# Optimization experiments

Measured on AMD Instinct MI355X. Metric: run time of the kernel, lower is better.

Reference implementation:

```python
import jax, jax.numpy as jnp
from jax import lax
import numpy as np

EPS = 1e-5
STRIDE = 4
K_NEIGHBORS = 16


def setup_inputs() -> dict:
    key = jax.random.key(0)
    ks = jax.random.split(key, 4)
    B, N, Cin, Cout = 16, 4096, 64, 128
    p1 = jax.random.normal(ks[0], (B, N, 3), dtype=jnp.float32)
    x1 = jax.random.normal(ks[1], (B, Cin, N), dtype=jnp.float32)
    w1 = jax.random.normal(ks[2], (Cout, Cin + 3), dtype=jnp.float32) * 0.05
    w2 = jax.random.normal(ks[3], (Cout, Cout), dtype=jnp.float32) * 0.05
    g1 = jnp.ones((Cout,), jnp.float32)
    b1 = jnp.zeros((Cout,), jnp.float32)
    g2 = jnp.ones((Cout,), jnp.float32)
    b2 = jnp.zeros((Cout,), jnp.float32)
    return {"p1": p1, "x1": x1, "w1": w1, "g1": g1, "b1": b1,
            "w2": w2, "g2": g2, "b2": b2}


def farthest_point_sampling(p, npoint):
    # p: [B, N, 3] -> centroids [B, npoint] (deterministic start at index 0)
    B, N, _ = p.shape
    gather_pt = jax.vmap(lambda pts, f: pts[f])  # [B,N,3],[B] -> [B,3]

    def step(carry, _):
        dist, farthest = carry
        centroid = gather_pt(p, farthest)                     # [B, 3]
        d = jnp.sum((p - centroid[:, None, :]) ** 2, -1)      # [B, N]
        dist = jnp.minimum(dist, d)
        new_far = jnp.argmax(dist, axis=-1).astype(jnp.int32)
        return (dist, new_far), farthest

    init = (jnp.full((B, N), 1e10, dtype=p.dtype), jnp.zeros((B,), jnp.int32))
    _, idxs = lax.scan(step, init, None, length=npoint)       # [npoint, B]
    return idxs.T                                             # [B, npoint]


def knn_point(k, xyz, new_xyz):
    # squared distances via gram trick; exclude all-zero points like the original
    n1 = jnp.sum(xyz ** 2, -1)                                # [B, N]
    n2 = jnp.sum(new_xyz ** 2, -1)                            # [B, M]
    d2 = n2[:, :, None] + n1[:, None, :] - 2.0 * jnp.einsum('bmc,bnc->bmn', new_xyz, xyz)
    zero_mask = jnp.all(xyz == 0, axis=-1)                    # [B, N]
    d2 = jnp.where(zero_mask[:, None, :], jnp.inf, d2)
    _, idx = lax.top_k(-d2, k)                                # smallest-k -> [B, M, k]
    return idx


def _bn_relu(h, g, b):
    # BatchNorm2d (training-mode batch stats, biased var) over (B, M, k) per channel
    m = jnp.mean(h, axis=(0, 1, 2), keepdims=True)
    v = jnp.mean((h - m) ** 2, axis=(0, 1, 2), keepdims=True)
    return jax.nn.relu(g * (h - m) * lax.rsqrt(v + EPS) + b)


def reference(p1, x1, w1, g1, b1, w2, g2, b2):
    B, N, _ = p1.shape
    M = max(1, N // STRIDE)
    k = K_NEIGHBORS

    idx = farthest_point_sampling(p1, M)                      # [B, M]
    gather2 = jax.vmap(lambda pts, i: pts[i])
    p2 = gather2(p1, idx)                                     # [B, M, 3]

    idx_knn = knn_point(k, p1, p2)                            # [B, M, k]
    grouped_p1 = gather2(p1, idx_knn)                         # [B, M, k, 3]
    xt = jnp.transpose(x1, (0, 2, 1))                         # [B, N, Cin]
    grouped_x1 = gather2(xt, idx_knn)                         # [B, M, k, Cin]

    rel = grouped_p1 - p2[:, :, None, :]                      # [B, M, k, 3]
    feats = jnp.concatenate([rel, grouped_x1], axis=-1)       # [B, M, k, 3+Cin]

    h = _bn_relu(jnp.einsum('bmkc,oc->bmko', feats, w1), g1, b1)
    h = _bn_relu(jnp.einsum('bmkc,oc->bmko', h, w2), g2, b2)
    new_features = jnp.max(h, axis=2)                         # maxpool over k -> [B, M, Cout]
    return p2, jnp.transpose(new_features, (0, 2, 1))         # ([B,M,3], [B,Cout,M])
```

## Files before the change

### kernel.cpp

```cpp
#include <hip/hip_runtime.h>
#include <hip/hip_bf16.h>
#include <hip/hip_cooperative_groups.h>
#include <cstdint>

namespace cg = cooperative_groups;

#define BB 16
#define NN 4096
#define MM 1024
#define KNB 16
#define CIN 64
#define COUT 128
#define RTOT (BB*MM*KNB)
#define AP1 104
#define AP2 136

typedef __attribute__((ext_vector_type(8))) short short8v;
typedef __attribute__((ext_vector_type(4))) float floatx4;
typedef __attribute__((ext_vector_type(2))) float f32x2;

__device__ __forceinline__ float bflo(uint32_t u){ return __uint_as_float(u << 16); }
__device__ __forceinline__ float bfhi(uint32_t u){ return __uint_as_float(u & 0xffff0000u); }
__device__ __forceinline__ uint32_t f2bf_pk(float a, float b){
  uint32_t ua = __float_as_uint(a), ub = __float_as_uint(b);
  ua += 0x7fffu + ((ua >> 16) & 1u);
  ub += 0x7fffu + ((ub >> 16) & 1u);
  return (ua >> 16) | (ub & 0xffff0000u);
}
__device__ __forceinline__ uint16_t f2bf1(float a){
  uint32_t u = __float_as_uint(a);
  u += 0x7fffu + ((u >> 16) & 1u);
  return (uint16_t)(u >> 16);
}
template<int CTRL>
__device__ __forceinline__ float dpp_f(float v){
  return __int_as_float(__builtin_amdgcn_update_dpp(__float_as_int(v), __float_as_int(v), CTRL, 0xf, 0xf, false));
}

struct FpsS { float pc[NN*3]; float4 sel[MM]; unsigned long long cand[2][8]; };
struct TrS  { float t[64][65]; };
struct ConsS{ uint16_t Bh1[128*AP1]; uint16_t AhD[128*AP2];
              int winq[8*16]; float ssum[128]; float ssq[128]; };
union PreU  { FpsS fps; TrS tr; ConsS cons; };

__global__ __launch_bounds__(512, 2) void k_pre2(
    const float* __restrict__ p1, const float* __restrict__ x1,
    const float* __restrict__ w1,
    float* __restrict__ outp2, float* __restrict__ p2w,
    float4* __restrict__ p1n, uint16_t* __restrict__ xtb, float* __restrict__ Sz,
    uint16_t* __restrict__ h1, float* __restrict__ S1,
    int* __restrict__ prog, int* __restrict__ prep_done)
{
  __shared__ PreU u;
  const int blk = blockIdx.x, tid = threadIdx.x;
  const int lane = tid & 63, wid = tid >> 6;

  if (blk < 16){
    int b = blk;
    const float* pb = p1 + (size_t)b*NN*3;
    float4 f[6];
    const float4* src = (const float4*)(pb + tid*24);
    #pragma unroll
    for (int j=0;j<6;j++) f[j] = src[j];
    #pragma unroll
    for (int j=0;j<6;j++) *(float4*)(u.fps.pc + tid*24 + j*4) = f[j];
    const float* fa = (const float*)f;
    f32x2 px2[4], py2[4], pz2[4], ds2[4];
    #pragma unroll
    for (int j=0;j<4;j++){
      px2[j][0]=fa[6*j+0]; px2[j][1]=fa[6*j+3];
      py2[j][0]=fa[6*j+1]; py2[j][1]=fa[6*j+4];
      pz2[j][0]=fa[6*j+2]; pz2[j][1]=fa[6*j+5];
      ds2[j][0]=1e10f;     ds2[j][1]=1e10f;
    }
    __syncthreads();
    float cx = u.fps.pc[0], cy = u.fps.pc[1], cz = u.fps.pc[2];
    if (tid==64) u.fps.sel[0] = make_float4(cx, cy, cz, 0.f);
    int g0 = tid*8;

    for (int i=1;i<MM;i++){
      f32x2 nd2[4];
      {
        #pragma clang fp contract(off)
        f32x2 cx2; cx2[0]=cx; cx2[1]=cx;
        f32x2 cy2; cy2[0]=cy; cy2[1]=cy;
        f32x2 cz2; cz2[0]=cz; cz2[1]=cz;
        #pragma unroll
        for (int j=0;j<4;j++){
          f32x2 dx = px2[j] - cx2;
          f32x2 dy = py2[j] - cy2;
          f32x2 dz = pz2[j] - cz2;
          f32x2 d  = dx*dx + dy*dy + dz*dz;
          f32x2 nd;
          nd[0] = fminf(ds2[j][0], d[0]);
          nd[1] = fminf(ds2[j][1], d[1]);
          nd2[j] = nd; ds2[j] = nd;
        }
      }
      float lm = fmaxf(fmaxf(fmaxf(nd2[0][0],nd2[0][1]), fmaxf(nd2[1][0],nd2[1][1])),
                       fmaxf(fmaxf(nd2[2][0],nd2[2][1]), fmaxf(nd2[3][0],nd2[3][1])));
      int li = g0+7;
      li = (nd2[3][0]==lm) ? g0+6 : li;
      li = (nd2[2][1]==lm) ? g0+5 : li;
      li = (nd2[2][0]==lm) ? g0+4 : li;
      li = (nd2[1][1]==lm) ? g0+3 : li;
      li = (nd2[1][0]==lm) ? g0+2 : li;
      li = (nd2[0][1]==lm) ? g0+1 : li;
      li = (nd2[0][0]==lm) ? g0+0 : li;
      float wm = lm;
      wm = fmaxf(wm, dpp_f<0xB1>(wm));
      wm = fmaxf(wm, dpp_f<0x4E>(wm));
      wm = fmaxf(wm, dpp_f<0x124>(wm));
      wm = fmaxf(wm, dpp_f<0x128>(wm));
      wm = fmaxf(wm, __int_as_float(__builtin_amdgcn_ds_swizzle(__float_as_int(wm), 0x401F)));
      wm = fmaxf(wm, __shfl_xor(wm, 32));
      unsigned long long bm = __ballot(lm == wm);
      int fl = __ffsll(bm) - 1;
      int wi = __builtin_amdgcn_readlane(li, fl);
      if (lane == 0)
        u.fps.cand[i&1][wid] = (((unsigned long long)(unsigned)__float_as_uint(wm)) << 32)
                               | (unsigned)(0xFFFFu ^ (unsigned)wi);
      __syncthreads();
      const unsigned long long* cd = u.fps.cand[i&1];
      unsigned long long c0=cd[0],c1=cd[1],c2=cd[2],c3=cd[3],c4=cd[4],c5=cd[5],c6=cd[6],c7=cd[7];
      unsigned long long a0 = c0>c1?c0:c1, a1 = c2>c3?c2:c3;
      unsigned long long a2 = c4>c5?c4:c5, a3 = c6>c7?c6:c7;
      unsigned long long b0 = a0>a1?a0:a1, b1 = a2>a3?a2:a3;
      unsigned long long mb = b0>b1?b0:b1;
      int midx = (int)(0xFFFFu ^ (unsigned)(mb & 0xFFFFull));
      cx = u.fps.pc[midx*3+0]; cy = u.fps.pc[midx*3+1]; cz = u.fps.pc[midx*3+2];
      if (tid==64) u.fps.sel[i] = make_float4(cx, cy, cz, 0.f);
      if ((i & 63) == 63 && wid == 1){
        int e = i - 63 + lane;
        float4 s = u.fps.sel[e];
        float n2 = __fadd_rn(__fadd_rn(__fmul_rn(s.x,s.x),__fmul_rn(s.y,s.y)),__fmul_rn(s.z,s.z));
        *(float4*)(p2w + ((size_t)b*MM + e)*4) = make_float4(s.x, s.y, s.z, n2);
        if (lane == 0)
          __hip_atomic_store(&prog[b*16], i+1, __ATOMIC_RELEASE, __HIP_MEMORY_SCOPE_AGENT);
      }
    }
    __syncthreads();
    for (int e = tid; e < MM; e += 512){
      float4 s = u.fps.sel[e];
      float* o = outp2 + ((size_t)b*MM + e)*3;
      o[0]=s.x; o[1]=s.y; o[2]=s.z;
    }
  } else {
    for (int i = (blk-16)*512 + tid; i < 16384; i += 240*512) Sz[i] = 0.f;
    for (int i = (blk-16)*512 + tid; i < BB*NN; i += 240*512){
      float x = p1[(size_t)i*3+0], y = p1[(size_t)i*3+1], z = p1[(size_t)i*3+2];
      float n = __fadd_rn(__fadd_rn(__fmul_rn(x,x),__fmul_rn(y,y)),__fmul_rn(z,z));
      p1n[i] = make_float4(x,y,z,n);
    }
    for (int tile = blk-16; tile < 1024; tile += 240){
      int b = tile >> 6, n0 = (tile & 63)*64;
      __syncthreads();
      int c = tid >> 3, q = tid & 7;
      const float* src = x1 + ((size_t)(b*64 + c))*NN + n0 + q*8;
      float4 f0 = *(const float4*)src, f1 = *(const float4*)(src+4);
      u.tr.t[c][q*8+0]=f0.x; u.tr.t[c][q*8+1]=f0.y; u.tr.t[c][q*8+2]=f0.z; u.tr.t[c][q*8+3]=f0.w;
      u.tr.t[c][q*8+4]=f1.x; u.tr.t[c][q*8+5]=f1.y; u.tr.t[c][q*8+6]=f1.z; u.tr.t[c][q*8+7]=f1.w;
      __syncthreads();
      int n = tid >> 3;
      uint32_t* dst = (uint32_t*)(xtb + ((size_t)(b*NN + n0 + n))*64 + q*8);
      #pragma unroll
      for (int j=0;j<4;j++)
        dst[j] = f2bf_pk(u.tr.t[q*8+2*j][n], u.tr.t[q*8+2*j+1][n]);
    }
    __threadfence();
    __syncthreads();
    if (tid == 0) atomicAdd(prep_done, 1);
    for (int e = tid; e < 128*96; e += 512){
      int o = e / 96, k = e - o*96;
      float v = (k < 64) ? w1[o*67 + 3 + k] : ((k < 67) ? w1[o*67 + (k-64)] : 0.f);
      u.cons.Bh1[o*AP1 + k] = f2bf1(v);
    }
    if (tid < 128){ u.cons.ssum[tid]=0.f; u.cons.ssq[tid]=0.f; }
    __syncthreads();
    {
      int pv = 0, sp = 0;
      if (lane == 0) pv = __hip_atomic_load(prep_done, __ATOMIC_ACQUIRE, __HIP_MEMORY_SCOPE_AGENT);
      pv = __shfl(pv, 0);
      while (pv < 240 && sp < (1<<16)){
        __builtin_amdgcn_s_sleep(64);
        if (lane == 0) pv = __hip_atomic_load(prep_done, __ATOMIC_ACQUIRE, __HIP_MEMORY_SCOPE_AGENT);
        pv = __shfl(pv, 0); sp++;
      }
    }
    int ml = lane & 15, quad = lane >> 4, seg = lane >> 4;
    int gw = (blk-16)*8 + wid;
    for (int qi = gw; qi < BB*MM; qi += 1920){
      int b = qi & 15, m = qi >> 4;
      int q2 = b*MM + m;
      {
        int pv = 0, sp = 0;
        if (lane == 0) pv = __hip_atomic_load(&prog[b*16], __ATOMIC_ACQUIRE, __HIP_MEMORY_SCOPE_AGENT);
        pv = __shfl(pv, 0);
        while (pv <= m && sp < (1<<16)){
          __builtin_amdgcn_s_sleep(64);
          if (lane == 0) pv = __hip_atomic_load(&prog[b*16], __ATOMIC_ACQUIRE, __HIP_MEMORY_SCOPE_AGENT);
          pv = __shfl(pv, 0); sp++;
        }
      }
      const float4 qv = *(const float4*)(p2w + (size_t)q2*4);
      const float4* pbn = p1n + (size_t)b*NN;
      float bd[16]; int bi[16];
      #pragma unroll
      for (int s=0;s<16;s++){ bd[s] = 1e30f; bi[s] = 0; }
      float wv = 1e30f; int wslot = 0;

      #define KPROC(T, PV) { \
        float dot = fmaf(qv.z, (PV).z, fmaf(qv.y, (PV).y, __fmul_rn(qv.x, (PV).x))); \
        float d2 = __fsub_rn(__fadd_rn(qv.w, (PV).w), __fmul_rn(2.0f, dot)); \
        if (d2 < wv){ \
          int c = (T)*64 + lane; \
          _Pragma("unroll") \
          for (int s=0;s<16;s++) if (s==wslot){ bd[s]=d2; bi[s]=c; } \
          wv = bd[0]; wslot = 0; \
          _Pragma("unroll") \
          for (int s=1;s<16;s++) if (bd[s] > wv){ wv = bd[s]; wslot = s; } \
        } }

      float4 cur = pbn[lane];
      for (int t=0;t<63;t++){
        float4 nx = pbn[(t+1)*64 + lane];
        KPROC(t, cur);
        cur = nx;
      }
      KPROC(63, cur);
      #undef KPROC

      float lv = bd[0]; int ls = 0;
      #pragma unroll
      for (int s=1;s<16;s++) if (bd[s] < lv){ lv = bd[s]; ls = s; }
      for (int r=0;r<16;r++){
        float rv = lv; int rl = lane;
        #pragma unroll
        for (int off=32; off>=1; off>>=1){
          float ov = __shfl_xor(rv, off); int ol = __shfl_xor(rl, off);
          if (ov < rv || (ov == rv && ol < rl)){ rv = ov; rl = ol; }
        }
        if (lane == rl){
          int idx = 0;
          #pragma unroll
          for (int s=0;s<16;s++) if (s==ls) idx = bi[s];
          u.cons.winq[wid*16 + r] = idx;
          #pragma unroll
          for (int s=0;s<16;s++) if (s==ls) bd[s] = 1e30f;
          lv = bd[0]; ls = 0;
          #pragma unroll
          for (int s=1;s<16;s++) if (bd[s] < lv){ lv = bd[s]; ls = s; }
        }
      }
      int n = u.cons.winq[wid*16 + ml];
      {
        const uint4* s4 = (const uint4*)(xtb + ((size_t)(b*NN + n))*64 + seg*16);
        uint4* d4 = (uint4*)(u.cons.AhD + (wid*16 + ml)*AP2 + seg*16);
        d4[0] = s4[0]; d4[1] = s4[1];
        if (seg == 0){
          const float* pp = p1 + ((size_t)(b*NN + n))*3;
          float rx = __fsub_rn(pp[0], qv.x);
          float ry = __fsub_rn(pp[1], qv.y);
          float rz = __fsub_rn(pp[2], qv.z);
          uint4* dr = (uint4*)(u.cons.AhD + (wid*16 + ml)*AP2 + 64);
          dr[0] = make_uint4(f2bf_pk(rx, ry), f2bf_pk(rz, 0.f), 0u, 0u);
          dr[1] = make_uint4(0u,0u,0u,0u);
          dr[2] = make_uint4(0u,0u,0u,0u);
          dr[3] = make_uint4(0u,0u,0u,0u);
        }
      }
      short8v af[3];
      #pragma unroll
      for (int kc=0;kc<3;kc++)
        af[kc] = *(const short8v*)(u.cons.AhD + (wid*16 + ml)*AP2 + kc*32 + quad*8);
      floatx4 acc[8];
      #pragma unroll
      for (int ct=0;ct<8;ct++) acc[ct] = (floatx4){0.f,0.f,0.f,0.f};
      #pragma unroll
      for (int ct=0;ct<8;ct++){
        #pragma unroll
        for (int kc=0;kc<3;kc++){
          short8v bf = *(const short8v*)(u.cons.Bh1 + (ct*16+ml)*AP1 + kc*32 + quad*8);
          acc[ct] = __builtin_amdgcn_mfma_f32_16x16x32_bf16(af[kc], bf, acc[ct], 0, 0, 0);
        }
      }
      float csum[8], csq[8];
      #pragma unroll
      for (int ct=0;ct<8;ct++){
        float a0=acc[ct][0], a1=acc[ct][1], a2=acc[ct][2], a3=acc[ct][3];
        float s = (a0+a1)+(a2+a3);
        float qq2 = (a0*a0+a1*a1)+(a2*a2+a3*a3);
        s += __shfl_xor(s,16);  s += __shfl_xor(s,32);
        qq2 += __shfl_xor(qq2,16); qq2 += __shfl_xor(qq2,32);
        csum[ct]=s; csq[ct]=qq2;
        #pragma unroll
        for (int r=0;r<4;r++)
          u.cons.AhD[(wid*16 + quad*4 + r)*AP2 + ct*16 + ml] = f2bf1(acc[ct][r]);
      }
      #pragma unroll
      for (int jj=0;jj<2;jj++){
        int ct = quad*2 + jj, col = ct*16 + ml;
        atomicAdd(&u.cons.ssum[col], csum[ct]);
        atomicAdd(&u.cons.ssq[col],  csq[ct]);
      }
      {
        const uint4* s4 = (const uint4*)(u.cons.AhD + (wid*16 + ml)*AP2 + seg*32);
        uint4* dst = (uint4*)(h1 + ((size_t)q2*16 + ml)*128 + seg*32);
        dst[0]=s4[0]; dst[1]=s4[1]; dst[2]=s4[2]; dst[3]=s4[3];
      }
    }
    __syncthreads();
    int cp = (blk & 31)*256;
    if (tid < 128){ atomicAdd(&S1[cp+tid], u.cons.ssum[tid]); atomicAdd(&S1[cp+128+tid], u.cons.ssq[tid]); }
  }
}

__global__ __launch_bounds__(256) void k_gemm2(const __hip_bfloat16* __restrict__ h1,
                                               const float* __restrict__ w2,
                                               const float* __restrict__ g1v, const float* __restrict__ b1v,
                                               const float* __restrict__ S1, float* __restrict__ S2,
                                               float* __restrict__ hmax, float* __restrict__ hmin){
  __shared__ __hip_bfloat16 Ah[64*AP2];
  __shared__ __hip_bfloat16 Bh[128*AP2];
  __shared__ float scb[128], shb[128], ssum[128], ssq[128];
  int tid = threadIdx.x;
  if (tid < 128){
    float s=0.f, q=0.f;
    for (int c=0;c<32;c++){ s += S1[c*256+tid]; q += S1[c*256+128+tid]; }
    float inv = 1.0f / (float)RTOT;
    float mean = s * inv;
    float var  = q * inv - mean*mean;
    float rs = 1.0f / sqrtf(var + 1e-5f);
    float scv = g1v[tid] * rs;
    scb[tid] = scv;
    shb[tid] = b1v[tid] - mean*scv;
    ssum[tid] = 0.f; ssq[tid] = 0.f;
  }
  {
    int o = tid >> 1, hf = tid & 1;
    const float4* wr = (const float4*)(w2 + (size_t)o*128 + hf*64);
    uint32_t* bd = (uint32_t*)(Bh + o*AP2 + hf*64);
    #pragma unroll
    for (int q=0;q<16;q++){
      float4 v = wr[q];
      bd[2*q]   = f2bf_pk(v.x, v.y);
      bd[2*q+1] = f2bf_pk(v.z, v.w);
    }
  }
  __syncthreads();
  int lane = tid & 63, wid = tid >> 6;
  int m0 = wid*16, ml = lane & 15, quad = lane >> 4;
  for (int j = 0; j < 4; j++){
    int tile = blockIdx.x*4 + j;
    int r0 = tile * 64;
    if (j) __syncthreads();
    {
      int row = tid >> 2, seg = tid & 3;
      const uint4* hp4 = (const uint4*)(h1 + ((size_t)(r0+row))*128 + seg*32);
      #pragma unroll
      for (int q=0;q<4;q++){
        uint4 u = hp4[q];
        int cg = seg*32 + q*8;
        uint32_t wv[4] = {u.x,u.y,u.z,u.w};
        uint32_t ov[4];
        #pragma unroll
        for (int t=0;t<4;t++){
          int c = cg + t*2;
          float a0 = fmaxf(fmaf(bflo(wv[t]), scb[c],   shb[c]),   0.f);
          float a1 = fmaxf(fmaf(bfhi(wv[t]), scb[c+1], shb[c+1]), 0.f);
          ov[t] = f2bf_pk(a0, a1);
        }
        *(uint4*)(Ah + row*AP2 + cg) = make_uint4(ov[0],ov[1],ov[2],ov[3]);
      }
    }
    __syncthreads();
    short8v af[4];
    #pragma unroll
    for (int kc=0;kc<4;kc++)
      af[kc] = *(const short8v*)(Ah + (m0+ml)*AP2 + kc*32 + quad*8);
    floatx4 acc[8];
    #pragma unroll
    for (int ct=0;ct<8;ct++) acc[ct] = (floatx4){0.f,0.f,0.f,0.f};
    #pragma unroll
    for (int ct=0;ct<8;ct++){
      #pragma unroll
      for (int kc=0;kc<4;kc++){
        short8v bf = *(const short8v*)(Bh + (ct*16+ml)*AP2 + kc*32 + quad*8);
        acc[ct] = __builtin_amdgcn_mfma_f32_16x16x32_bf16(af[kc], bf, acc[ct], 0, 0, 0);
      }
    }
    int mrow = (r0 >> 4) + wid;
    float cm[8], cn[8], cs[8], cq[8];
    #pragma unroll
    for (int ct=0;ct<8;ct++){
      float a0=acc[ct][0], a1=acc[ct][1], a2=acc[ct][2], a3=acc[ct][3];
      float mx = fmaxf(fmaxf(a0,a1), fmaxf(a2,a3));
      float mn = fminf(fminf(a0,a1), fminf(a2,a3));
      float s  = (a0+a1)+(a2+a3);
      float q2 = (a0*a0+a1*a1)+(a2*a2+a3*a3);
      mx = fmaxf(mx, __shfl_xor(mx,16)); mx = fmaxf(mx, __shfl_xor(mx,32));
      mn = fminf(mn, __shfl_xor(mn,16)); mn = fminf(mn, __shfl_xor(mn,32));
      s += __shfl_xor(s,16);  s += __shfl_xor(s,32);
      q2 += __shfl_xor(q2,16); q2 += __shfl_xor(q2,32);
      cm[ct]=mx; cn[ct]=mn; cs[ct]=s; cq[ct]=q2;
    }
    #pragma unroll
    for (int jj=0;jj<2;jj++){
      int ct = quad*2 + jj, col = ct*16 + ml;
      hmax[(size_t)mrow*128 + col] = cm[ct];
      hmin[(size_t)mrow*128 + col] = cn[ct];
      atomicAdd(&ssum[col], cs[ct]);
      atomicAdd(&ssq[col],  cq[ct]);
    }
  }
  __syncthreads();
  int cp = (blockIdx.x & 31)*256;
  if (tid < 128){ atomicAdd(&S2[cp+tid], ssum[tid]); atomicAdd(&S2[cp+128+tid], ssq[tid]); }
}

__global__ __launch_bounds__(256) void k_pool(const float* __restrict__ hmax, const float* __restrict__ hmin,
                                              const float* __restrict__ g2v, const float* __restrict__ b2v,
                                              const float* __restrict__ S2, float* __restrict__ out1){
  __shared__ float ot[128*65];
  __shared__ float scs[128], shs[128];
  int tid = threadIdx.x, blk = blockIdx.x;
  int b = blk >> 4, m0 = (blk & 15) * 64;
  if (tid < 128){
    float s=0.f, q=0.f;
    for (int c=0;c<32;c++){ s += S2[c*256+tid]; q += S2[c*256+128+tid]; }
    float inv = 1.0f / (float)RTOT;
    float mean = s * inv;
    float var  = q * inv - mean*mean;
    float rs = 1.0f / sqrtf(var + 1e-5f);
    float scv = g2v[tid] * rs;
    scs[tid] = scv;
    shs[tid] = b2v[tid] - mean*scv;
  }
  __syncthreads();
  int ml = tid >> 2, oq = tid & 3, o0 = oq*32;
  int gm = b*MM + m0 + ml;
  const float4* xr = (const float4*)(hmax + (size_t)gm*128 + o0);
  const float4* nr = (const float4*)(hmin + (size_t)gm*128 + o0);
  #pragma unroll
  for (int j2=0;j2<8;j2++){
    float4 hx = xr[j2], hn = nr[j2];
    float hv[4] = {hx.x, hx.y, hx.z, hx.w};
    float nv[4] = {hn.x, hn.y, hn.z, hn.w};
    #pragma unroll
    for (int e=0;e<4;e++){
      int c = o0 + j2*4 + e;
      float sc = scs[c], sh = shs[c];
      float h = (sc >= 0.f) ? hv[e] : nv[e];
      ot[c*65 + ml] = fmaxf(fmaf(h, sc, sh), 0.f);
    }
  }
  __syncthreads();
  int o = tid >> 1, mh = tid & 1;
  float* dst = out1 + ((size_t)(b*COUT + o))*MM + m0 + mh*32;
  #pragma unroll
  for (int j2=0;j2<8;j2++){
    float4 v;
    v.x=ot[o*65+mh*32+j2*4+0]; v.y=ot[o*65+mh*32+j2*4+1];
    v.z=ot[o*65+mh*32+j2*4+2]; v.w=ot[o*65+mh*32+j2*4+3];
    *(float4*)(dst + j2*4) = v;
  }
}

extern "C" void kernel_launch(void* const* d_in, const int* in_sizes, int n_in,
                              void* d_out, int out_size, void* d_ws, size_t ws_size,
                              hipStream_t stream) {
  (void)in_sizes; (void)n_in; (void)out_size; (void)ws_size;
  const float* p1 = (const float*)d_in[0];
  const float* x1 = (const float*)d_in[1];
  const float* w1 = (const float*)d_in[2];
  const float* g1 = (const float*)d_in[3];
  const float* b1 = (const float*)d_in[4];
  const float* w2 = (const float*)d_in[5];
  const float* g2 = (const float*)d_in[6];
  const float* b2 = (const float*)d_in[7];
  float* out = (float*)d_out;
  float* ws  = (float*)d_ws;

  uint16_t* xtb = (uint16_t*)ws;
  float4* p1n   = (float4*)(ws + 2097152);
  float*  p2w   = ws + 2621440;
  float*  S1    = ws + 2686976;
  float*  S2    = ws + 2695168;
  uint16_t* h1  = (uint16_t*)(ws + 2703872);
  float*  hmax  = ws + 19481088;
  float*  hmin  = ws + 21578240;
  int*    prog  = (int*)(ws + 23675392);
  int*    prep_done = (int*)(ws + 23675392) + 256;
  float*  outp2 = out;
  float*  out1  = out + 49152;

  hipMemsetAsync(prog, 0, 2048, stream);

  void* args[] = { (void*)&p1, (void*)&x1, (void*)&w1,
                   (void*)&outp2, (void*)&p2w,
                   (void*)&p1n, (void*)&xtb, (void*)&S1,
                   (void*)&h1, (void*)&S1, (void*)&prog, (void*)&prep_done };
  hipLaunchCooperativeKernel((void*)k_pre2, dim3(256), dim3(512), args, 0, stream);

  k_gemm2<<<1024, 256, 0, stream>>>((const __hip_bfloat16*)h1, w2, g1, b1, S1, S2, hmax, hmin);
  k_pool<<<256, 256, 0, stream>>>(hmax, hmin, g2, b2, S2, out1);
}
```

Measured before the change: 900.3 us.

## Run FPS on four waves with 16 points per lane and dedicated publisher wave

```diff
diff --git a/kernel.cpp b/kernel.cpp
--- a/kernel.cpp
+++ b/kernel.cpp
@@ -18,6 +18,7 @@
 typedef __attribute__((ext_vector_type(8))) short short8v;
 typedef __attribute__((ext_vector_type(4))) float floatx4;
 typedef __attribute__((ext_vector_type(2))) float f32x2;
+typedef __attribute__((ext_vector_type(2))) unsigned int uint2v;
 
 __device__ __forceinline__ float bflo(uint32_t u){ return __uint_as_float(u << 16); }
 __device__ __forceinline__ float bfhi(uint32_t u){ return __uint_as_float(u & 0xffff0000u); }
@@ -36,8 +37,24 @@
 __device__ __forceinline__ float dpp_f(float v){
   return __int_as_float(__builtin_amdgcn_update_dpp(__float_as_int(v), __float_as_int(v), CTRL, 0xf, 0xf, false));
 }
-
-struct FpsS { float pc[NN*3]; float4 sel[MM]; unsigned long long cand[2][8]; };
+__device__ __forceinline__ float plmax16(float v){
+#if __has_builtin(__builtin_amdgcn_permlane16_swap)
+  uint2v r = __builtin_amdgcn_permlane16_swap(__float_as_uint(v), __float_as_uint(v), false, false);
+  return fmaxf(__uint_as_float(r[0]), __uint_as_float(r[1]));
+#else
+  return fmaxf(v, __int_as_float(__builtin_amdgcn_ds_swizzle(__float_as_int(v), 0x401F)));
+#endif
+}
+__device__ __forceinline__ float plmax32(float v){
+#if __has_builtin(__builtin_amdgcn_permlane32_swap)
+  uint2v r = __builtin_amdgcn_permlane32_swap(__float_as_uint(v), __float_as_uint(v), false, false);
+  return fmaxf(__uint_as_float(r[0]), __uint_as_float(r[1]));
+#else
+  return fmaxf(v, __shfl_xor(v, 32));
+#endif
+}
+
+struct FpsS { float4 pcv[NN]; float4 sel[MM]; unsigned long long candk[2][4]; };
 struct TrS  { float t[64][65]; };
 struct ConsS{ uint16_t Bh1[128*AP1]; uint16_t AhD[128*AP2];
               int winq[8*16]; float ssum[128]; float ssq[128]; };
@@ -58,88 +75,107 @@
   if (blk < 16){
     int b = blk;
     const float* pb = p1 + (size_t)b*NN*3;
-    float4 f[6];
-    const float4* src = (const float4*)(pb + tid*24);
-    #pragma unroll
-    for (int j=0;j<6;j++) f[j] = src[j];
-    #pragma unroll
-    for (int j=0;j<6;j++) *(float4*)(u.fps.pc + tid*24 + j*4) = f[j];
-    const float* fa = (const float*)f;
-    f32x2 px2[4], py2[4], pz2[4], ds2[4];
-    #pragma unroll
-    for (int j=0;j<4;j++){
-      px2[j][0]=fa[6*j+0]; px2[j][1]=fa[6*j+3];
-      py2[j][0]=fa[6*j+1]; py2[j][1]=fa[6*j+4];
-      pz2[j][0]=fa[6*j+2]; pz2[j][1]=fa[6*j+5];
-      ds2[j][0]=1e10f;     ds2[j][1]=1e10f;
+    {
+      float4 f[6];
+      const float4* src = (const float4*)(pb + tid*24);
+      #pragma unroll
+      for (int j=0;j<6;j++) f[j] = src[j];
+      const float* fa = (const float*)f;
+      #pragma unroll
+      for (int j=0;j<8;j++)
+        u.fps.pcv[tid*8 + j] = make_float4(fa[3*j], fa[3*j+1], fa[3*j+2], 0.f);
     }
     __syncthreads();
-    float cx = u.fps.pc[0], cy = u.fps.pc[1], cz = u.fps.pc[2];
+    float4 c00 = u.fps.pcv[0];
+    float cx = c00.x, cy = c00.y, cz = c00.z;
     if (tid==64) u.fps.sel[0] = make_float4(cx, cy, cz, 0.f);
-    int g0 = tid*8;
+
+    f32x2 px2[8] = {}, py2[8] = {}, pz2[8] = {}, ds2[8] = {};
+    const int g0 = tid*16;
+    if (wid < 4){
+      #pragma unroll
+      for (int j=0;j<8;j++){
+        float4 a = u.fps.pcv[g0 + 2*j];
+        float4 bq = u.fps.pcv[g0 + 2*j + 1];
+        px2[j][0]=a.x; px2[j][1]=bq.x;
+        py2[j][0]=a.y; py2[j][1]=bq.y;
+        pz2[j][0]=a.z; pz2[j][1]=bq.z;
+        ds2[j][0]=1e10f; ds2[j][1]=1e10f;
+      }
+    }
 
     for (int i=1;i<MM;i++){
-      f32x2 nd2[4];
-      {
-        #pragma clang fp contract(off)
-        f32x2 cx2; cx2[0]=cx; cx2[1]=cx;
-        f32x2 cy2; cy2[0]=cy; cy2[1]=cy;
-        f32x2 cz2; cz2[0]=cz; cz2[1]=cz;
+      if (wid < 4){
+        {
+          #pragma clang fp contract(off)
+          f32x2 cx2; cx2[0]=cx; cx2[1]=cx;
+          f32x2 cy2; cy2[0]=cy; cy2[1]=cy;
+          f32x2 cz2; cz2[0]=cz; cz2[1]=cz;
+          #pragma unroll
+          for (int j=0;j<8;j++){
+            f32x2 dx = px2[j] - cx2;
+            f32x2 dy = py2[j] - cy2;
+            f32x2 dz = pz2[j] - cz2;
+            f32x2 d  = dx*dx + dy*dy + dz*dz;
+            ds2[j] = __builtin_elementwise_min(ds2[j], d);
+          }
+        }
+        f32x2 t0 = __builtin_elementwise_max(ds2[0], ds2[1]);
+        f32x2 t1 = __builtin_elementwise_max(ds2[2], ds2[3]);
+        f32x2 t2 = __builtin_elementwise_max(ds2[4], ds2[5]);
+        f32x2 t3 = __builtin_elementwise_max(ds2[6], ds2[7]);
+        f32x2 u0 = __builtin_elementwise_max(t0, t1);
+        f32x2 u1 = __builtin_elementwise_max(t2, t3);
+        f32x2 vv = __builtin_elementwise_max(u0, u1);
+        float lm = fmaxf(vv[0], vv[1]);
+        int li = g0 + 15;
         #pragma unroll
-        for (int j=0;j<4;j++){
-          f32x2 dx = px2[j] - cx2;
-          f32x2 dy = py2[j] - cy2;
-          f32x2 dz = pz2[j] - cz2;
-          f32x2 d  = dx*dx + dy*dy + dz*dz;
-          f32x2 nd;
-          nd[0] = fminf(ds2[j][0], d[0]);
-          nd[1] = fminf(ds2[j][1], d[1]);
-          nd2[j] = nd; ds2[j] = nd;
-        }
-      }
-      float lm = fmaxf(fmaxf(fmaxf(nd2[0][0],nd2[0][1]), fmaxf(nd2[1][0],nd2[1][1])),
-                       fmaxf(fmaxf(nd2[2][0],nd2[2][1]), fmaxf(nd2[3][0],nd2[3][1])));
-      int li = g0+7;
-      li = (nd2[3][0]==lm) ? g0+6 : li;
-      li = (nd2[2][1]==lm) ? g0+5 : li;
-      li = (nd2[2][0]==lm) ? g0+4 : li;
-      li = (nd2[1][1]==lm) ? g0+3 : li;
-      li = (nd2[1][0]==lm) ? g0+2 : li;
-      li = (nd2[0][1]==lm) ? g0+1 : li;
-      li = (nd2[0][0]==lm) ? g0+0 : li;
-      float wm = lm;
-      wm = fmaxf(wm, dpp_f<0xB1>(wm));
-      wm = fmaxf(wm, dpp_f<0x4E>(wm));
-      wm = fmaxf(wm, dpp_f<0x124>(wm));
-      wm = fmaxf(wm, dpp_f<0x128>(wm));
-      wm = fmaxf(wm, __int_as_float(__builtin_amdgcn_ds_swizzle(__float_as_int(wm), 0x401F)));
-      wm = fmaxf(wm, __shfl_xor(wm, 32));
-      unsigned long long bm = __ballot(lm == wm);
-      int fl = __ffsll(bm) - 1;
-      int wi = __builtin_amdgcn_readlane(li, fl);
-      if (lane == 0)
-        u.fps.cand[i&1][wid] = (((unsigned long long)(unsigned)__float_as_uint(wm)) << 32)
-                               | (unsigned)(0xFFFFu ^ (unsigned)wi);
+        for (int j=14;j>=0;j--){
+          float ev = ds2[j>>1][j & 1];
+          li = (ev == lm) ? (g0 + j) : li;
+        }
+        float wm = lm;
+        wm = fmaxf(wm, dpp_f<0xB1>(wm));
+        wm = fmaxf(wm, dpp_f<0x4E>(wm));
+        wm = fmaxf(wm, dpp_f<0x124>(wm));
+        wm = fmaxf(wm, dpp_f<0x128>(wm));
+        wm = plmax16(wm);
+        wm = plmax32(wm);
+        unsigned long long bmask = __ballot(lm == wm);
+        int fl = __ffsll(bmask) - 1;
+        int wi = __builtin_amdgcn_readlane(li, fl);
+        if (lane == 0)
+          u.fps.candk[i&1][wid] = (((unsigned long long)(unsigned)__float_as_uint(wm)) << 32)
+                                   | (unsigned)(0xFFFFu ^ (unsigned)wi);
+      }
       __syncthreads();
-      const unsigned long long* cd = u.fps.cand[i&1];
-      unsigned long long c0=cd[0],c1=cd[1],c2=cd[2],c3=cd[3],c4=cd[4],c5=cd[5],c6=cd[6],c7=cd[7];
-      unsigned long long a0 = c0>c1?c0:c1, a1 = c2>c3?c2:c3;
-      unsigned long long a2 = c4>c5?c4:c5, a3 = c6>c7?c6:c7;
-      unsigned long long b0 = a0>a1?a0:a1, b1 = a2>a3?a2:a3;
-      unsigned long long mb = b0>b1?b0:b1;
-      int midx = (int)(0xFFFFu ^ (unsigned)(mb & 0xFFFFull));
-      cx = u.fps.pc[midx*3+0]; cy = u.fps.pc[midx*3+1]; cz = u.fps.pc[midx*3+2];
-      if (tid==64) u.fps.sel[i] = make_float4(cx, cy, cz, 0.f);
-      if ((i & 63) == 63 && wid == 1){
-        int e = i - 63 + lane;
+      if (wid < 4){
+        const unsigned long long* cd = u.fps.candk[i&1];
+        unsigned long long cq0=cd[0], cq1=cd[1], cq2=cd[2], cq3=cd[3];
+        unsigned long long a0 = cq0>cq1?cq0:cq1, a1 = cq2>cq3?cq2:cq3;
+        unsigned long long mb = a0>a1?a0:a1;
+        int midx = (int)(0xFFFFu ^ (unsigned)(mb & 0xFFFFull));
+        float4 cv = u.fps.pcv[midx];
+        cx = cv.x; cy = cv.y; cz = cv.z;
+        if (tid==64) u.fps.sel[i] = make_float4(cx, cy, cz, 0.f);
+      } else if (wid == 4 && (i & 63) == 0){
+        int e = i - 64 + lane;
         float4 s = u.fps.sel[e];
         float n2 = __fadd_rn(__fadd_rn(__fmul_rn(s.x,s.x),__fmul_rn(s.y,s.y)),__fmul_rn(s.z,s.z));
         *(float4*)(p2w + ((size_t)b*MM + e)*4) = make_float4(s.x, s.y, s.z, n2);
         if (lane == 0)
-          __hip_atomic_store(&prog[b*16], i+1, __ATOMIC_RELEASE, __HIP_MEMORY_SCOPE_AGENT);
+          __hip_atomic_store(&prog[b*16], i, __ATOMIC_RELEASE, __HIP_MEMORY_SCOPE_AGENT);
       }
     }
     __syncthreads();
+    if (wid == 4){
+      int e = 960 + lane;
+      float4 s = u.fps.sel[e];
+      float n2 = __fadd_rn(__fadd_rn(__fmul_rn(s.x,s.x),__fmul_rn(s.y,s.y)),__fmul_rn(s.z,s.z));
+      *(float4*)(p2w + ((size_t)b*MM + e)*4) = make_float4(s.x, s.y, s.z, n2);
+      if (lane == 0)
+        __hip_atomic_store(&prog[b*16], MM, __ATOMIC_RELEASE, __HIP_MEMORY_SCOPE_AGENT);
+    }
     for (int e = tid; e < MM; e += 512){
       float4 s = u.fps.sel[e];
       float* o = outp2 + ((size_t)b*MM + e)*3;
```

After: 864.1 us. -4.0%, faster.
